# Optimization experiments

Measured on AMD Instinct MI355X. Metric: run time of the kernel, lower is better.

Reference implementation:

```python
import jax, jax.numpy as jnp
import numpy as np
from jax.scipy.special import digamma

N = 8192
DX = 16
DY = 16
BLK = 128  # row-block size for blocked pairwise Chebyshev distances
EPS = 1e-15  # original code subtracts 1e15 (obvious sign/typo bug -> empty balls, digamma(0)=-inf); intended tiny epsilon


def _cheb_block(blk, pts):
    # blk: [B, d], pts: [N, d] -> [B, N] Chebyshev (L-inf) distances
    return jnp.max(jnp.abs(blk[:, None, :] - pts[None, :, :]), axis=-1)


def _kth_topk_dist(pts, k):
    # For each row i: k-th value of torch.topk(dist[i], k) (k-th LARGEST, as in the source)
    nb = pts.shape[0] // BLK
    def body(_, blk):
        d = _cheb_block(blk, pts)               # [BLK, N]
        v = jax.lax.top_k(d, k)[0][:, -1]       # k-th largest distance
        return None, v
    _, vals = jax.lax.scan(body, None, pts.reshape(nb, BLK, pts.shape[1]))
    return vals.reshape(-1)                      # [N]


def _range_count(pts, radii):
    # count of points within L-inf radius radii[i] of pts[i] (inclusive, like cKDTree.query_ball_point p=inf)
    nb = pts.shape[0] // BLK
    def body(_, xs):
        blk, r = xs
        d = _cheb_block(blk, pts)               # [BLK, N]
        return None, jnp.sum(d <= r[:, None], axis=1)
    _, cnt = jax.lax.scan(body, None, (pts.reshape(nb, BLK, pts.shape[1]), radii.reshape(nb, BLK)))
    return cnt.reshape(-1)                       # [N] int


def setup_inputs() -> dict:
    key = jax.random.key(0)
    kx, ky = jax.random.split(key)
    return {
        "x_samples": jax.random.normal(kx, (N, DX), dtype=jnp.float32),
        "y_samples": jax.random.normal(ky, (N, DY), dtype=jnp.float32),
        "k": 4,
    }


def reference(x_samples, y_samples, k):
    n = x_samples.shape[0]
    dx = x_samples.shape[1]
    dy = y_samples.shape[1]
    data = jnp.concatenate([x_samples, y_samples], axis=1)  # [N, dx+dy]

    knn_dis = _kth_topk_dist(data, k)                        # [N]
    radii = knn_dis - EPS
    nx = _range_count(x_samples, radii).astype(jnp.float32)  # ball counts in X marginal
    ny = _range_count(y_samples, radii).astype(jnp.float32)  # ball counts in Y marginal

    log2 = jnp.log(jnp.float32(2.0))
    mean_log_r = jnp.mean(jnp.log(knn_dis))
    dig_n = digamma(jnp.float32(n))

    ans_xy = -digamma(jnp.float32(k)) + dig_n + (dx + dy) * log2 + (dx + dy) * mean_log_r
    ans_x = dig_n + dx * log2 - jnp.mean(digamma(nx)) + dx * mean_log_r
    ans_y = dig_n + dy * log2 - jnp.mean(digamma(ny)) + dy * mean_log_r
    return ans_x + ans_y - ans_xy
```

## Files before the change

kernel.cpp:

```cpp
#include <hip/hip_runtime.h>
#include <math.h>

#define NPTS 8192
#define TPB  256
#define TPM  256
#define QPB_M 32
#define NCHUNK 8
#define NC_MAX 256
#define NSPLIT 8
#define CPS 32

__device__ __forceinline__ float fmax3(float a, float b, float c) {
    return fmaxf(fmaxf(a, b), c);
}

__device__ __forceinline__ float max3abs(float a, float b, float c) {
    float r;
    asm("v_max3_f32 %0, |%1|, |%2|, |%3|" : "=v"(r) : "v"(a), "v"(b), "v"(c));
    return r;
}
__device__ __forceinline__ float max3vaa(float m, float b, float c) {
    float r;
    asm("v_max3_f32 %0, %1, |%2|, |%3|" : "=v"(r) : "v"(m), "v"(b), "v"(c));
    return r;
}
__device__ __forceinline__ float max3v(float a, float b, float c) {
    float r;
    asm("v_max3_f32 %0, %1, %2, %3" : "=v"(r) : "v"(a), "v"(b), "v"(c));
    return r;
}

__device__ __forceinline__ float cheb32_pair(const float* __restrict__ q,
                                             const float* __restrict__ p) {
    float s[32];
    #pragma unroll
    for (int k = 0; k < 32; ++k) s[k] = q[k] - p[k];
    float l[10];
    #pragma unroll
    for (int g = 0; g < 10; ++g) l[g] = max3abs(s[3*g], s[3*g+1], s[3*g+2]);
    float c3 = max3vaa(l[9], s[30], s[31]);
    float c0 = max3v(l[0], l[1], l[2]);
    float c1 = max3v(l[3], l[4], l[5]);
    float c2 = max3v(l[6], l[7], l[8]);
    return fmaxf(max3v(c0, c1, c2), c3);
}

__device__ __forceinline__ void ins4p(float d, int di,
    float& t0, float& t1, float& t2, float& t3,
    int& i0, int& i1, int& i2)
{
    bool c0 = d > t0;
    float v1 = fminf(t0, d); int j1 = c0 ? i0 : di;
    t0 = fmaxf(t0, d);       i0 = c0 ? di : i0;
    bool c1 = v1 > t1;
    float v2 = fminf(t1, v1); int j2 = c1 ? i1 : j1;
    t1 = fmaxf(t1, v1);       i1 = c1 ? j1 : i1;
    bool c2 = v2 > t2;
    float v3 = fminf(t2, v2);
    t2 = fmaxf(t2, v2);       i2 = c2 ? j2 : i2;
    t3 = fmaxf(t3, v3);
}

__device__ __forceinline__ void ins4full(float d, int di,
    float& t0, float& t1, float& t2, float& t3,
    int& i0, int& i1, int& i2, int& i3)
{
    bool c0 = d > t0;
    float v1 = fminf(t0, d); int j1 = c0 ? i0 : di;
    t0 = fmaxf(t0, d);       i0 = c0 ? di : i0;
    bool c1 = v1 > t1;
    float v2 = fminf(t1, v1); int j2 = c1 ? i1 : j1;
    t1 = fmaxf(t1, v1);       i1 = c1 ? j1 : i1;
    bool c2 = v2 > t2;
    float v3 = fminf(t2, v2); int j3 = c2 ? i2 : j2;
    t2 = fmaxf(t2, v2);       i2 = c2 ? j2 : i2;
    bool c3 = v3 > t3;
    t3 = fmaxf(t3, v3);       i3 = c3 ? j3 : i3;
}

__device__ double digamma_d(double x) {
    double r = 0.0;
    while (x < 6.0) { r -= 1.0 / x; x += 1.0; }
    double f = 1.0 / (x * x);
    double t = f * (1.0/12.0 - f * (1.0/120.0 - f * (1.0/252.0 - f * (1.0/240.0 - f * (1.0/132.0)))));
    return r + log(x) - 0.5 / x - t;
}

__device__ __forceinline__ void load_query(float* qv, const float* __restrict__ x,
                                           const float* __restrict__ y, int q)
{
    const float4* qx4 = reinterpret_cast<const float4*>(x) + (size_t)q * 4;
    const float4* qy4 = reinterpret_cast<const float4*>(y) + (size_t)q * 4;
    #pragma unroll
    for (int i = 0; i < 4; ++i) {
        float4 v = qx4[i];
        qv[4*i+0] = v.x; qv[4*i+1] = v.y; qv[4*i+2] = v.z; qv[4*i+3] = v.w;
        float4 w = qy4[i];
        qv[16+4*i+0] = w.x; qv[16+4*i+1] = w.y; qv[16+4*i+2] = w.z; qv[16+4*i+3] = w.w;
    }
}

__global__ __launch_bounds__(256) void extremes_kernel(
    const float* __restrict__ x, const float* __restrict__ y,
    unsigned short* __restrict__ cand_raw)
{
    const int dim  = blockIdx.x;
    const int tid  = threadIdx.x;
    const int lane = tid & 63;
    const int wave = tid >> 6;
    const float* base = (dim < 16) ? (x + dim) : (y + (dim - 16));

    float h0=-3.4e38f,h1=-3.4e38f,h2=-3.4e38f,h3=-3.4e38f;
    int   a0=0,a1=0,a2=0,a3=0;
    float l0=-3.4e38f,l1=-3.4e38f,l2=-3.4e38f,l3=-3.4e38f;
    int   b0=0,b1=0,b2=0,b3=0;
    #pragma unroll 8
    for (int j = tid; j < NPTS; j += 256) {
        float v = base[(size_t)j * 16];
        ins4full( v, j, h0,h1,h2,h3, a0,a1,a2,a3);
        ins4full(-v, j, l0,l1,l2,l3, b0,b1,b2,b3);
    }
    #pragma unroll
    for (int off = 32; off > 0; off >>= 1) {
        float m0=__shfl_xor(h0,off), m1=__shfl_xor(h1,off),
              m2=__shfl_xor(h2,off), m3=__shfl_xor(h3,off);
        int   c0=__shfl_xor(a0,off), c1=__shfl_xor(a1,off),
              c2=__shfl_xor(a2,off), c3=__shfl_xor(a3,off);
        ins4full(m0,c0, h0,h1,h2,h3, a0,a1,a2,a3);
        ins4full(m1,c1, h0,h1,h2,h3, a0,a1,a2,a3);
        ins4full(m2,c2, h0,h1,h2,h3, a0,a1,a2,a3);
        ins4full(m3,c3, h0,h1,h2,h3, a0,a1,a2,a3);
        float n0=__shfl_xor(l0,off), n1=__shfl_xor(l1,off),
              n2=__shfl_xor(l2,off), n3=__shfl_xor(l3,off);
        int   d0=__shfl_xor(b0,off), d1=__shfl_xor(b1,off),
              d2=__shfl_xor(b2,off), d3=__shfl_xor(b3,off);
        ins4full(n0,d0, l0,l1,l2,l3, b0,b1,b2,b3);
        ins4full(n1,d1, l0,l1,l2,l3, b0,b1,b2,b3);
        ins4full(n2,d2, l0,l1,l2,l3, b0,b1,b2,b3);
        ins4full(n3,d3, l0,l1,l2,l3, b0,b1,b2,b3);
    }
    __shared__ float shv[4][8];
    __shared__ int   shi[4][8];
    if (lane == 0) {
        shv[wave][0]=h0; shv[wave][1]=h1; shv[wave][2]=h2; shv[wave][3]=h3;
        shv[wave][4]=l0; shv[wave][5]=l1; shv[wave][6]=l2; shv[wave][7]=l3;
        shi[wave][0]=a0; shi[wave][1]=a1; shi[wave][2]=a2; shi[wave][3]=a3;
        shi[wave][4]=b0; shi[wave][5]=b1; shi[wave][6]=b2; shi[wave][7]=b3;
    }
    __syncthreads();
    if (tid == 0) {
        #pragma unroll
        for (int w = 1; w < 4; ++w) {
            #pragma unroll
            for (int e = 0; e < 4; ++e) {
                ins4full(shv[w][e],   shi[w][e],   h0,h1,h2,h3, a0,a1,a2,a3);
                ins4full(shv[w][4+e], shi[w][4+e], l0,l1,l2,l3, b0,b1,b2,b3);
            }
        }
        cand_raw[dim*8+0] = (unsigned short)a0;
        cand_raw[dim*8+1] = (unsigned short)a1;
        cand_raw[dim*8+2] = (unsigned short)a2;
        cand_raw[dim*8+3] = (unsigned short)a3;
        cand_raw[dim*8+4] = (unsigned short)b0;
        cand_raw[dim*8+5] = (unsigned short)b1;
        cand_raw[dim*8+6] = (unsigned short)b2;
        cand_raw[dim*8+7] = (unsigned short)b3;
    }
}

__global__ __launch_bounds__(256) void dedupe_kernel(
    const unsigned short* __restrict__ cand_raw,
    unsigned short* __restrict__ dlist)
{
    __shared__ unsigned mask[NPTS / 32];
    __shared__ unsigned short tmp[NC_MAX];
    __shared__ int cnt;
    const int tid = threadIdx.x;
    mask[tid] = 0;
    if (tid == 0) cnt = 0;
    __syncthreads();
    const int idx = cand_raw[tid];
    const unsigned bit = 1u << (idx & 31);
    unsigned old = atomicOr(&mask[idx >> 5], bit);
    if (!(old & bit)) { int p = atomicAdd(&cnt, 1); tmp[p] = (unsigned short)idx; }
    __syncthreads();
    dlist[tid] = (tid < cnt) ? tmp[tid] : (unsigned short)0xFFFF;
}

__global__ __launch_bounds__(TPB, 2) void knn_cand_kernel(
    const float* __restrict__ x, const float* __restrict__ y,
    const unsigned short* __restrict__ dlist,
    float4* __restrict__ part_v, ushort4* __restrict__ part_i)
{
    __shared__ float pc[CPS * 32];
    __shared__ unsigned short scidx[CPS];
    const int tid = threadIdx.x;
    if (tid < CPS) scidx[tid] = dlist[blockIdx.y * CPS + tid];
    __syncthreads();
    #pragma unroll
    for (int it = 0; it < (CPS * 32) / TPB; ++it) {
        int e = it * TPB + tid;
        int cand = e >> 5, dim = e & 31;
        int ci = scidx[cand];
        int j = (ci == 0xFFFF) ? 0 : ci;
        pc[e] = (dim < 16) ? x[(size_t)j * 16 + dim] : y[(size_t)j * 16 + dim - 16];
    }
    const int q = blockIdx.x * TPB + tid;
    float qv[32];
    load_query(qv, x, y, q);
    float t0=-1.f,t1=-1.f,t2=-1.f,t3=-1.f;
    int i0=0,i1=0,i2=0;
    __syncthreads();
    for (int jj = 0; jj < CPS; ++jj) {
        int ci = scidx[jj];
        if (ci == 0xFFFF) break;
        float m = cheb32_pair(qv, pc + jj * 32);
        ins4p(m, ci, t0, t1, t2, t3, i0, i1, i2);
    }
    part_v[(size_t)blockIdx.y * NPTS + q] = make_float4(t0, t1, t2, t3);
    part_i[(size_t)blockIdx.y * NPTS + q] =
        make_ushort4((unsigned short)i0, (unsigned short)i1, (unsigned short)i2, 0);
}

template <int CL>
__global__ __launch_bounds__(TPM) void merge_check_kernel(
    const float4* __restrict__ part_v, const ushort4* __restrict__ part_i,
    const float* __restrict__ x, const float* __restrict__ y,
    double* __restrict__ acc)
{
    __shared__ float4  sv[NCHUNK][QPB_M];
    __shared__ ushort4 si[NCHUNK][QPB_M];
    const int ql = threadIdx.x & (QPB_M - 1);
    const int ck = threadIdx.x / QPB_M;
    const int q  = blockIdx.x * QPB_M + ql;

    float t0=-1.f,t1=-1.f,t2=-1.f,t3=-1.f;
    int i0=0,i1=0,i2=0;
    #pragma unroll
    for (int k = 0; k < CL; ++k) {
        const int s = ck * CL + k;
        float4  v  = part_v[(size_t)s * NPTS + q];
        ushort4 id = part_i[(size_t)s * NPTS + q];
        ins4p(v.x, id.x, t0,t1,t2,t3, i0,i1,i2);
        ins4p(v.y, id.y, t0,t1,t2,t3, i0,i1,i2);
        ins4p(v.z, id.z, t0,t1,t2,t3, i0,i1,i2);
        ins4p(v.w, 0,    t0,t1,t2,t3, i0,i1,i2);
    }
    sv[ck][ql] = make_float4(t0, t1, t2, t3);
    si[ck][ql] = make_ushort4((unsigned short)i0, (unsigned short)i1,
                              (unsigned short)i2, 0);
    __syncthreads();

    if (ck == 0) {
        #pragma unroll
        for (int c = 1; c < NCHUNK; ++c) {
            float4  v  = sv[c][ql];
            ushort4 id = si[c][ql];
            ins4p(v.x, id.x, t0,t1,t2,t3, i0,i1,i2);
            ins4p(v.y, id.y, t0,t1,t2,t3, i0,i1,i2);
            ins4p(v.z, id.z, t0,t1,t2,t3, i0,i1,i2);
            ins4p(v.w, 0,    t0,t1,t2,t3, i0,i1,i2);
        }
        const float rq = t3 - 1e-15f;

        float qv[32];
        load_query(qv, x, y, q);

        float vals[3] = { t0, t1, t2 };
        int   idxs[3] = { i0, i1, i2 };
        int missx = 0, missy = 0;
        #pragma unroll
        for (int k = 0; k < 3; ++k) {
            const int j = idxs[k];
            const float4* px4 = reinterpret_cast<const float4*>(x) + (size_t)j * 4;
            const float4* py4 = reinterpret_cast<const float4*>(y) + (size_t)j * 4;
            float mx = 0.0f, my = 0.0f;
            #pragma unroll
            for (int i = 0; i < 4; ++i) {
                float4 a = px4[i];
                mx = fmax3(mx, fmax3(fabsf(qv[4*i+0]-a.x), fabsf(qv[4*i+1]-a.y),
                                     fabsf(qv[4*i+2]-a.z)), fabsf(qv[4*i+3]-a.w));
                float4 b = py4[i];
                my = fmax3(my, fmax3(fabsf(qv[16+4*i+0]-b.x), fabsf(qv[16+4*i+1]-b.y),
                                     fabsf(qv[16+4*i+2]-b.z)), fabsf(qv[16+4*i+3]-b.w));
            }
            const bool act = vals[k] > rq;
            missx += (act && (mx > rq)) ? 1 : 0;
            missy += (act && (my > rq)) ? 1 : 0;
        }
        const int nx = NPTS - missx;
        const int ny = NPTS - missy;
        double d = digamma_d((double)nx) + digamma_d((double)ny);
        #pragma unroll
        for (int off = 16; off > 0; off >>= 1)
            d += __shfl_down(d, off, 32);
        if (ql == 0) atomicAdd(acc, d);
    }
}

__global__ __launch_bounds__(64) void final_kernel(
    const double* __restrict__ acc, float* __restrict__ out)
{
    if (threadIdx.x == 0) {
        double ans = digamma_d((double)NPTS) + digamma_d(4.0) - acc[0] / (double)NPTS;
        out[0] = (float)ans;
    }
}

extern "C" void kernel_launch(void* const* d_in, const int* in_sizes, int n_in,
                              void* d_out, int out_size, void* d_ws, size_t ws_size,
                              hipStream_t stream)
{
    (void)in_sizes; (void)n_in; (void)out_size; (void)ws_size;
    const float* x = (const float*)d_in[0];
    const float* y = (const float*)d_in[1];
    float* out = (float*)d_out;

    char* ws = (char*)d_ws;
    double* acc = (double*)ws;
    unsigned short* cand_raw = (unsigned short*)(ws + 16);
    unsigned short* dlist    = (unsigned short*)(ws + 528);
    float4*  part_v = (float4*)(ws + 1040);
    ushort4* part_i = (ushort4*)(ws + 1040 + (size_t)NSPLIT * NPTS * 16);

    hipMemsetAsync(acc, 0, sizeof(double), stream);
    extremes_kernel<<<32, 256, 0, stream>>>(x, y, cand_raw);
    dedupe_kernel<<<1, 256, 0, stream>>>(cand_raw, dlist);
    knn_cand_kernel<<<dim3(NPTS / TPB, NSPLIT), TPB, 0, stream>>>(x, y, dlist,
                                                                  part_v, part_i);
    merge_check_kernel<1><<<NPTS / QPB_M, TPM, 0, stream>>>(part_v, part_i, x, y, acc);
    final_kernel<<<1, 64, 0, stream>>>(acc, out);
}
```

Baseline: 87.70 us.

## Fuse candidate kNN scan and merge-check into one kernel, drop memset

```diff
diff --git a/kernel.cpp b/kernel.cpp
--- a/kernel.cpp
+++ b/kernel.cpp
@@ -3,12 +3,10 @@
 
 #define NPTS 8192
 #define TPB  256
-#define TPM  256
-#define QPB_M 32
-#define NCHUNK 8
 #define NC_MAX 256
-#define NSPLIT 8
-#define CPS 32
+#define QPB  64
+#define NCH  4
+#define CPC  64
 
 __device__ __forceinline__ float fmax3(float a, float b, float c) {
     return fmaxf(fmaxf(a, b), c);
@@ -102,12 +100,13 @@
 
 __global__ __launch_bounds__(256) void extremes_kernel(
     const float* __restrict__ x, const float* __restrict__ y,
-    unsigned short* __restrict__ cand_raw)
+    unsigned short* __restrict__ cand_raw, double* __restrict__ acc)
 {
     const int dim  = blockIdx.x;
     const int tid  = threadIdx.x;
     const int lane = tid & 63;
     const int wave = tid >> 6;
+    if (dim == 0 && tid == 0) acc[0] = 0.0;
     const float* base = (dim < 16) ? (x + dim) : (y + (dim - 16));
 
     float h0=-3.4e38f,h1=-3.4e38f,h2=-3.4e38f,h3=-3.4e38f;
@@ -187,65 +186,42 @@
     dlist[tid] = (tid < cnt) ? tmp[tid] : (unsigned short)0xFFFF;
 }
 
-__global__ __launch_bounds__(TPB, 2) void knn_cand_kernel(
+__global__ __launch_bounds__(TPB) void cand_check_kernel(
     const float* __restrict__ x, const float* __restrict__ y,
-    const unsigned short* __restrict__ dlist,
-    float4* __restrict__ part_v, ushort4* __restrict__ part_i)
-{
-    __shared__ float pc[CPS * 32];
-    __shared__ unsigned short scidx[CPS];
+    const unsigned short* __restrict__ dlist, double* __restrict__ acc)
+{
+    __shared__ float pc[NC_MAX * 32];
+    __shared__ unsigned short scidx[NC_MAX];
+    __shared__ float4  sv[NCH][QPB];
+    __shared__ ushort4 si[NCH][QPB];
     const int tid = threadIdx.x;
-    if (tid < CPS) scidx[tid] = dlist[blockIdx.y * CPS + tid];
-    __syncthreads();
-    #pragma unroll
-    for (int it = 0; it < (CPS * 32) / TPB; ++it) {
+    const int ql  = tid & (QPB - 1);
+    const int ck  = tid >> 6;
+    const int q   = blockIdx.x * QPB + ql;
+
+    scidx[tid] = dlist[tid];
+    __syncthreads();
+    #pragma unroll
+    for (int it = 0; it < (NC_MAX * 32) / TPB; ++it) {
         int e = it * TPB + tid;
         int cand = e >> 5, dim = e & 31;
         int ci = scidx[cand];
         int j = (ci == 0xFFFF) ? 0 : ci;
         pc[e] = (dim < 16) ? x[(size_t)j * 16 + dim] : y[(size_t)j * 16 + dim - 16];
     }
-    const int q = blockIdx.x * TPB + tid;
+
     float qv[32];
     load_query(qv, x, y, q);
     float t0=-1.f,t1=-1.f,t2=-1.f,t3=-1.f;
     int i0=0,i1=0,i2=0;
     __syncthreads();
-    for (int jj = 0; jj < CPS; ++jj) {
+
+    for (int jj = ck * CPC; jj < ck * CPC + CPC; ++jj) {
         int ci = scidx[jj];
         if (ci == 0xFFFF) break;
         float m = cheb32_pair(qv, pc + jj * 32);
         ins4p(m, ci, t0, t1, t2, t3, i0, i1, i2);
     }
-    part_v[(size_t)blockIdx.y * NPTS + q] = make_float4(t0, t1, t2, t3);
-    part_i[(size_t)blockIdx.y * NPTS + q] =
-        make_ushort4((unsigned short)i0, (unsigned short)i1, (unsigned short)i2, 0);
-}
-
-template <int CL>
-__global__ __launch_bounds__(TPM) void merge_check_kernel(
-    const float4* __restrict__ part_v, const ushort4* __restrict__ part_i,
-    const float* __restrict__ x, const float* __restrict__ y,
-    double* __restrict__ acc)
-{
-    __shared__ float4  sv[NCHUNK][QPB_M];
-    __shared__ ushort4 si[NCHUNK][QPB_M];
-    const int ql = threadIdx.x & (QPB_M - 1);
-    const int ck = threadIdx.x / QPB_M;
-    const int q  = blockIdx.x * QPB_M + ql;
-
-    float t0=-1.f,t1=-1.f,t2=-1.f,t3=-1.f;
-    int i0=0,i1=0,i2=0;
-    #pragma unroll
-    for (int k = 0; k < CL; ++k) {
-        const int s = ck * CL + k;
-        float4  v  = part_v[(size_t)s * NPTS + q];
-        ushort4 id = part_i[(size_t)s * NPTS + q];
-        ins4p(v.x, id.x, t0,t1,t2,t3, i0,i1,i2);
-        ins4p(v.y, id.y, t0,t1,t2,t3, i0,i1,i2);
-        ins4p(v.z, id.z, t0,t1,t2,t3, i0,i1,i2);
-        ins4p(v.w, 0,    t0,t1,t2,t3, i0,i1,i2);
-    }
     sv[ck][ql] = make_float4(t0, t1, t2, t3);
     si[ck][ql] = make_ushort4((unsigned short)i0, (unsigned short)i1,
                               (unsigned short)i2, 0);
@@ -253,7 +229,7 @@
 
     if (ck == 0) {
         #pragma unroll
-        for (int c = 1; c < NCHUNK; ++c) {
+        for (int c = 1; c < NCH; ++c) {
             float4  v  = sv[c][ql];
             ushort4 id = si[c][ql];
             ins4p(v.x, id.x, t0,t1,t2,t3, i0,i1,i2);
@@ -262,9 +238,6 @@
             ins4p(v.w, 0,    t0,t1,t2,t3, i0,i1,i2);
         }
         const float rq = t3 - 1e-15f;
-
-        float qv[32];
-        load_query(qv, x, y, q);
 
         float vals[3] = { t0, t1, t2 };
         int   idxs[3] = { i0, i1, i2 };
@@ -292,8 +265,8 @@
         const int ny = NPTS - missy;
         double d = digamma_d((double)nx) + digamma_d((double)ny);
         #pragma unroll
-        for (int off = 16; off > 0; off >>= 1)
-            d += __shfl_down(d, off, 32);
+        for (int off = 32; off > 0; off >>= 1)
+            d += __shfl_down(d, off, 64);
         if (ql == 0) atomicAdd(acc, d);
     }
 }
@@ -320,14 +293,9 @@
     double* acc = (double*)ws;
     unsigned short* cand_raw = (unsigned short*)(ws + 16);
     unsigned short* dlist    = (unsigned short*)(ws + 528);
-    float4*  part_v = (float4*)(ws + 1040);
-    ushort4* part_i = (ushort4*)(ws + 1040 + (size_t)NSPLIT * NPTS * 16);
-
-    hipMemsetAsync(acc, 0, sizeof(double), stream);
-    extremes_kernel<<<32, 256, 0, stream>>>(x, y, cand_raw);
+
+    extremes_kernel<<<32, 256, 0, stream>>>(x, y, cand_raw, acc);
     dedupe_kernel<<<1, 256, 0, stream>>>(cand_raw, dlist);
-    knn_cand_kernel<<<dim3(NPTS / TPB, NSPLIT), TPB, 0, stream>>>(x, y, dlist,
-                                                                  part_v, part_i);
-    merge_check_kernel<1><<<NPTS / QPB_M, TPM, 0, stream>>>(part_v, part_i, x, y, acc);
+    cand_check_kernel<<<NPTS / QPB, TPB, 0, stream>>>(x, y, dlist, acc);
     final_kernel<<<1, 64, 0, stream>>>(acc, out);
 }
```

Measured after the change: 92.09 us. +5.0%, slower.
